# Kernel tuning notes

Measured on AMD Instinct MI355X. Metric: run time of the kernel, lower is better.

The kernel has to match this reference:

```python
import jax, jax.numpy as jnp
import numpy as np

BIG_NUMBER = 1e7   # repo constant used to mask padded adjacency slots
MAX_ITERS = 32     # params['flow_iters']


def _build_graph(B, N, D, valid_deg, seed=0):
    """Random d-regular-ish graph: each valid slot d holds a permutation of nodes,
    so every node has exactly `valid_deg` in-edges. in_indices[b,v,d] = (b,u,s)
    such that adj[b,u,s] == v. Padded slots (d >= valid_deg) hold the sentinel N
    and their in_indices point to a padded (near-zero-weight) flow entry."""
    rng = np.random.default_rng(seed)
    adj = np.full((B, N, D), N, dtype=np.int32)
    in_idx = np.zeros((B, N, D, 3), dtype=np.int32)
    in_idx[..., 0] = np.arange(B, dtype=np.int32)[:, None, None]
    in_idx[..., 2] = valid_deg  # padded slots -> flow[b, 0, valid_deg] (weight ~ 0)
    for b in range(B):
        for d in range(valid_deg):
            perm = rng.permutation(N).astype(np.int32)
            adj[b, :, d] = perm                      # edge u -> perm[u] via slot d
            inv = np.argsort(perm).astype(np.int32)  # inv[v] = u with perm[u] == v
            in_idx[b, :, d, 1] = inv
            in_idx[b, :, d, 2] = d
    return jnp.asarray(adj), jnp.asarray(in_idx)


def setup_inputs():
    B, N, D, VALID = 4, 100000, 16, 12
    key = jax.random.key(0)
    k1, k2 = jax.random.split(key)
    adj_lst, in_indices = _build_graph(B, N, D, VALID)
    return {
        "flow_proportions": jax.random.normal(k1, (B, N, D), dtype=jnp.float32),
        "demands": jax.random.normal(k2, (B, N, 1), dtype=jnp.float32),
        "adj_lst": adj_lst,
        "in_indices": in_indices,
        "num_nodes": N,
    }


def reference(flow_proportions, demands, adj_lst, in_indices, num_nodes):
    # --- masked softmax over neighbor slots (padded slots get -BIG_NUMBER) ---
    mask = (adj_lst == num_nodes).astype(flow_proportions.dtype)   # [B,N,D]
    masked = flow_proportions - BIG_NUMBER * mask
    weights = jax.nn.softmax(masked, axis=-1)                      # normalized_weights

    # --- mcf_solver: iterate flow <- weights * relu(inflow - demand) ---
    bidx = in_indices[..., 0]   # [B,N,D] batch index
    src = in_indices[..., 1]    # [B,N,D] source node of d-th in-edge
    slot = in_indices[..., 2]   # [B,N,D] slot of this node in source's adj list

    def step(flow, _):
        # gather incoming edge flows, sum -> inflow per node [B,N,1]
        inflow = flow[bidx, src, slot].sum(axis=-1, keepdims=True)
        new_flow = weights * jax.nn.relu(inflow - demands)
        return new_flow, None

    flow, _ = jax.lax.scan(step, jnp.zeros_like(weights), None, length=MAX_ITERS)
    # flow_cost (loss) = sum over nodes/slots of cost_fn(flow) = flow**2 here:
    # flow_cost = jnp.sum(flow * flow, axis=(1, 2))
    return flow
```

## Files before the change

### kernel.cpp

```cpp
#include <hip/hip_runtime.h>

#define DEG 16
#define MAX_ITERS 32
#define BLK_F 1024
#define GRID_F 256

__device__ __forceinline__ void grid_barrier(unsigned* cnt, unsigned* gen,
                                             unsigned target, unsigned nblocks) {
    __syncthreads();
    if (threadIdx.x == 0) {
        __threadfence();
        unsigned arrived = __hip_atomic_fetch_add(cnt, 1u, __ATOMIC_ACQ_REL,
                                                  __HIP_MEMORY_SCOPE_AGENT);
        if (arrived == nblocks - 1u) {
            __hip_atomic_store(cnt, 0u, __ATOMIC_RELAXED, __HIP_MEMORY_SCOPE_AGENT);
            __hip_atomic_fetch_add(gen, 1u, __ATOMIC_RELEASE, __HIP_MEMORY_SCOPE_AGENT);
        } else {
            while (__hip_atomic_load(gen, __ATOMIC_RELAXED,
                                     __HIP_MEMORY_SCOPE_AGENT) < target) {
                __builtin_amdgcn_s_sleep(2);
            }
        }
        __threadfence();
    }
    __syncthreads();
}

__device__ __forceinline__ void softmax_row(const float* __restrict__ fp,
                                            const int* __restrict__ adj,
                                            float* __restrict__ wout,
                                            size_t base, int N) {
    const float4* f4 = (const float4*)(fp + base);
    const int4*   a4 = (const int4*)(adj + base);
    float v[DEG];
#pragma unroll
    for (int k = 0; k < DEG / 4; ++k) {
        float4 f = f4[k];
        int4   a = a4[k];
        v[4*k+0] = (a.x == N) ? f.x - 1e7f : f.x;
        v[4*k+1] = (a.y == N) ? f.y - 1e7f : f.y;
        v[4*k+2] = (a.z == N) ? f.z - 1e7f : f.z;
        v[4*k+3] = (a.w == N) ? f.w - 1e7f : f.w;
    }
    float m = v[0];
#pragma unroll
    for (int j = 1; j < DEG; ++j) m = fmaxf(m, v[j]);
    float s = 0.f;
#pragma unroll
    for (int j = 0; j < DEG; ++j) { v[j] = __expf(v[j] - m); s += v[j]; }
    float inv = 1.f / s;
    float4* w4 = (float4*)(wout + base);
#pragma unroll
    for (int k = 0; k < DEG / 4; ++k) {
        float4 o;
        o.x = v[4*k+0] * inv;
        o.y = v[4*k+1] * inv;
        o.z = v[4*k+2] * inv;
        o.w = v[4*k+3] * inv;
        w4[k] = o;
    }
}

__device__ __forceinline__ void load_edges(const int* __restrict__ in_idx,
                                           const float* __restrict__ wsrc,
                                           int n, int N,
                                           int* __restrict__ src,
                                           float* __restrict__ w) {
    const int4* t4 = (const int4*)(in_idx + 3 * (size_t)n * DEG);
#pragma unroll
    for (int g = 0; g < 4; ++g) {
        int4 qa = t4[3*g + 0];
        int4 qb = t4[3*g + 1];
        int4 qc = t4[3*g + 2];
        int b0 = qa.x, s0 = qa.y, l0 = qa.z;
        int b1 = qa.w, s1 = qb.x, l1 = qb.y;
        int b2 = qb.z, s2 = qb.w, l2 = qc.x;
        int b3 = qc.y, s3 = qc.z, l3 = qc.w;
        int f0 = b0 * N + s0, f1 = b1 * N + s1;
        int f2 = b2 * N + s2, f3 = b3 * N + s3;
        src[4*g+0] = f0; src[4*g+1] = f1; src[4*g+2] = f2; src[4*g+3] = f3;
        w[4*g+0] = wsrc[(size_t)f0 * DEG + l0];
        w[4*g+1] = wsrc[(size_t)f1 * DEG + l1];
        w[4*g+2] = wsrc[(size_t)f2 * DEG + l2];
        w[4*g+3] = wsrc[(size_t)f3 * DEG + l3];
    }
}

__global__ __launch_bounds__(BLK_F, 4)
void fused3_k(const float* __restrict__ fp, const int* __restrict__ adj,
              const int* __restrict__ in_idx, const float* __restrict__ dem,
              const int* __restrict__ nn, float* __restrict__ wout,
              float* __restrict__ Ra, float* __restrict__ Rb,
              unsigned* __restrict__ bar_cnt, unsigned* __restrict__ bar_gen,
              int nodes) {
    const int N = *nn;
    const unsigned nb = gridDim.x;
    unsigned bar = 0;

    int start, end;
    if (nodes == 4 * N && nb == GRID_F) {
        int batch = (blockIdx.x & 7) >> 1;
        int rank  = ((blockIdx.x >> 3) << 1) | (blockIdx.x & 1);
        int per   = (N + 63) >> 6;
        int bend  = batch * N + N;
        start = batch * N + rank * per;
        end   = start + per;
        if (end > bend) end = bend;
        if (start > bend) start = bend;
    } else {
        int per = (nodes + nb - 1) / nb;
        start = blockIdx.x * per;
        end   = start + per;
        if (end > nodes) end = nodes;
        if (start > nodes) start = nodes;
    }

    const int n0 = start + (int)threadIdx.x;
    const int n1 = start + (int)threadIdx.x + BLK_F;
    const bool a0 = (n0 < end);
    const bool a1 = (n1 < end);
    const size_t b0 = (size_t)n0 * DEG, b1 = (size_t)n1 * DEG;

    if (a0) softmax_row(fp, adj, wout, b0, N);
    if (a1) softmax_row(fp, adj, wout, b1, N);
    grid_barrier(bar_cnt, bar_gen, ++bar, nb);

    int   src0[DEG], src1[DEG];
    float w0[DEG],   w1[DEG];
    float d0 = 0.f, d1 = 0.f;
#pragma unroll
    for (int k = 0; k < DEG; ++k) { src0[k] = 0; w0[k] = 0.f; src1[k] = 0; w1[k] = 0.f; }
    if (a0) { d0 = dem[n0]; load_edges(in_idx, wout, n0, N, src0, w0); }
    if (a1) { d1 = dem[n1]; load_edges(in_idx, wout, n1, N, src1, w1); }

    unsigned skipA = 0, skipB = 0;
#pragma unroll
    for (int k = 0; k < DEG; ++k) {
        if (__ballot(w0[k] != 0.f) == 0ull) skipA |= (1u << k);
        if (__ballot(w1[k] != 0.f) == 0ull) skipB |= (1u << k);
    }
    const unsigned sk0 = __builtin_amdgcn_readfirstlane(skipA);
    const unsigned sk1 = __builtin_amdgcn_readfirstlane(skipB);

    float r0 = fmaxf(-d0, 0.f), r1 = fmaxf(-d1, 0.f);
    if (a0) Ra[n0] = r0;
    if (a1) Ra[n1] = r1;
    grid_barrier(bar_cnt, bar_gen, ++bar, nb);

    const float* Rin = Ra;
    float*       Rout = Rb;
    for (int t = 1; t < MAX_ITERS; ++t) {
        float acc0 = 0.f, acc1 = 0.f;
        if (a0) {
#pragma unroll
            for (int k = 0; k < DEG; ++k)
                if (!((sk0 >> k) & 1u)) acc0 += w0[k] * Rin[src0[k]];
        }
        if (a1) {
#pragma unroll
            for (int k = 0; k < DEG; ++k)
                if (!((sk1 >> k) & 1u)) acc1 += w1[k] * Rin[src1[k]];
        }
        r0 = fmaxf(acc0 - d0, 0.f);
        r1 = fmaxf(acc1 - d1, 0.f);
        if (t < MAX_ITERS - 1) {
            if (a0) Rout[n0] = r0;
            if (a1) Rout[n1] = r1;
            grid_barrier(bar_cnt, bar_gen, ++bar, nb);
            float* tmp = (float*)Rin; Rin = Rout; Rout = tmp;
        }
    }

    if (a0) {
        float4* w4 = (float4*)(wout + b0);
#pragma unroll
        for (int k = 0; k < DEG / 4; ++k) {
            float4 v = w4[k];
            v.x *= r0; v.y *= r0; v.z *= r0; v.w *= r0;
            w4[k] = v;
        }
    }
    if (a1) {
        float4* w4 = (float4*)(wout + b1);
#pragma unroll
        for (int k = 0; k < DEG / 4; ++k) {
            float4 v = w4[k];
            v.x *= r1; v.y *= r1; v.z *= r1; v.w *= r1;
            w4[k] = v;
        }
    }
}

__global__ void softmax_k(const float* __restrict__ fp, const int* __restrict__ adj,
                          const int* __restrict__ nn, float* __restrict__ wout,
                          int nodes) {
    int i = blockIdx.x * blockDim.x + threadIdx.x;
    if (i >= nodes) return;
    softmax_row(fp, adj, wout, (size_t)i * DEG, *nn);
}

__global__ void gather_k(const int* __restrict__ in_idx, const float* __restrict__ w,
                         const int* __restrict__ nn, int* __restrict__ e_src,
                         float* __restrict__ e_w, int edges) {
    int e = blockIdx.x * blockDim.x + threadIdx.x;
    if (e >= edges) return;
    const int N = *nn;
    size_t e3 = 3 * (size_t)e;
    int fi = in_idx[e3] * N + in_idx[e3 + 1];
    e_src[e] = fi;
    e_w[e]   = w[(size_t)fi * DEG + in_idx[e3 + 2]];
}

__global__ void iter_k(const int* __restrict__ e_src, const float* __restrict__ e_w,
                       const float* __restrict__ dem, const float* __restrict__ Rin,
                       float* __restrict__ Rout, int nodes) {
    int i = blockIdx.x * blockDim.x + threadIdx.x;
    if (i >= nodes) return;
    const size_t base = (size_t)i * DEG;
    const int4*   s4 = (const int4*)(e_src + base);
    const float4* w4 = (const float4*)(e_w + base);
    float acc = 0.f;
#pragma unroll
    for (int k = 0; k < DEG / 4; ++k) {
        int4   s = s4[k];
        float4 w = w4[k];
        acc += w.x * Rin[s.x];
        acc += w.y * Rin[s.y];
        acc += w.z * Rin[s.z];
        acc += w.w * Rin[s.w];
    }
    float r = acc - dem[i];
    Rout[i] = r > 0.f ? r : 0.f;
}

__global__ void final_k(const float* __restrict__ w, const float* __restrict__ R,
                        float* __restrict__ out, int nodes) {
    int i = blockIdx.x * blockDim.x + threadIdx.x;
    if (i >= nodes) return;
    float r = R[i];
    const size_t base = (size_t)i * DEG;
    const float4* w4 = (const float4*)(w + base);
    float4* o4 = (float4*)(out + base);
#pragma unroll
    for (int k = 0; k < DEG / 4; ++k) {
        float4 v = w4[k];
        v.x *= r; v.y *= r; v.z *= r; v.w *= r;
        o4[k] = v;
    }
}

extern "C" void kernel_launch(void* const* d_in, const int* in_sizes, int n_in,
                              void* d_out, int out_size, void* d_ws, size_t ws_size,
                              hipStream_t stream) {
    const float* fp  = (const float*)d_in[0];
    const float* dem = (const float*)d_in[1];
    const int*   adj = (const int*)d_in[2];
    const int*   idx = (const int*)d_in[3];
    const int*   nn  = (const int*)d_in[4];

    const int edges = in_sizes[0];
    const int nodes = in_sizes[1];

    float* weights = (float*)d_out;

    char* ws = (char*)d_ws;
    unsigned* bar_cnt = (unsigned*)ws;
    unsigned* bar_gen = (unsigned*)(ws + 128);
    int*   e_src = (int*)ws;
    float* e_w   = (float*)(ws + (size_t)edges * sizeof(int));
    float* R0    = (float*)(ws + (size_t)edges * sizeof(int) + (size_t)edges * sizeof(float));
    float* R1    = R0 + nodes;

    int dev = 0, cus = 0, maxBlk = 0;
    hipGetDevice(&dev);
    hipDeviceGetAttribute(&cus, hipDeviceAttributeMultiprocessorCount, dev);
    hipOccupancyMaxActiveBlocksPerMultiprocessor(&maxBlk, (const void*)fused3_k,
                                                 BLK_F, 0);

    const int per_blk = (nodes + GRID_F - 1) / GRID_F;

    if (maxBlk >= 1 && cus >= GRID_F && per_blk <= 2 * BLK_F) {
        hipMemsetAsync(ws, 0, 256, stream);
        void* args[] = { (void*)&fp, (void*)&adj, (void*)&idx, (void*)&dem,
                         (void*)&nn, (void*)&weights, (void*)&R0, (void*)&R1,
                         (void*)&bar_cnt, (void*)&bar_gen, (void*)&nodes };
        hipLaunchCooperativeKernel((const void*)fused3_k, dim3(GRID_F), dim3(BLK_F),
                                   args, 0, stream);
    } else {
        const int blk = 256;
        const int gn = (nodes + blk - 1) / blk;
        const int ge = (edges + blk - 1) / blk;
        hipMemsetAsync(R0, 0, (size_t)nodes * sizeof(float), stream);
        softmax_k<<<gn, blk, 0, stream>>>(fp, adj, nn, weights, nodes);
        gather_k<<<ge, blk, 0, stream>>>(idx, weights, nn, e_src, e_w, edges);
        float* a = R0;
        float* b = R1;
        for (int t = 0; t < MAX_ITERS; ++t) {
            iter_k<<<gn, blk, 0, stream>>>(e_src, e_w, dem, a, b, nodes);
            float* tmp = a; a = b; b = tmp;
        }
        final_k<<<gn, blk, 0, stream>>>(weights, a, (float*)d_out, nodes);
    }
}
```

Baseline: 1.029 ms.

## Stage residual vector in LDS chunks instead of random global gathers

Each iteration, the block now cooperatively streams the range of R spanned by its in-edge sources into shared memory in 16K-float chunks, then resolves each edge's gather from LDS. Zero-weight edges are marked with a sentinel, and each thread's edges are bitonic-sorted. The block computes its min/max source range so only the chunks it needs are loaded. This trades scattered global/L2 gathers for coalesced streaming plus extra syncthreads and per-chunk range checks. Random permutation graphs make each block touch nearly its whole batch of R every iteration.

```diff
diff --git a/kernel.cpp b/kernel.cpp
--- a/kernel.cpp
+++ b/kernel.cpp
@@ -4,6 +4,9 @@
 #define MAX_ITERS 32
 #define BLK_F 1024
 #define GRID_F 256
+#define CHUNK_LOG 14
+#define CHUNK (1 << CHUNK_LOG)
+#define SENTINEL 0x7FFFFFFF
 
 __device__ __forceinline__ void grid_barrier(unsigned* cnt, unsigned* gen,
                                              unsigned target, unsigned nblocks) {
@@ -72,12 +75,10 @@
         int4 qa = t4[3*g + 0];
         int4 qb = t4[3*g + 1];
         int4 qc = t4[3*g + 2];
-        int b0 = qa.x, s0 = qa.y, l0 = qa.z;
-        int b1 = qa.w, s1 = qb.x, l1 = qb.y;
-        int b2 = qb.z, s2 = qb.w, l2 = qc.x;
-        int b3 = qc.y, s3 = qc.z, l3 = qc.w;
-        int f0 = b0 * N + s0, f1 = b1 * N + s1;
-        int f2 = b2 * N + s2, f3 = b3 * N + s3;
+        int f0 = qa.x * N + qa.y;  int l0 = qa.z;
+        int f1 = qa.w * N + qb.x;  int l1 = qb.y;
+        int f2 = qb.z * N + qb.w;  int l2 = qc.x;
+        int f3 = qc.y * N + qc.z;  int l3 = qc.w;
         src[4*g+0] = f0; src[4*g+1] = f1; src[4*g+2] = f2; src[4*g+3] = f3;
         w[4*g+0] = wsrc[(size_t)f0 * DEG + l0];
         w[4*g+1] = wsrc[(size_t)f1 * DEG + l1];
@@ -86,13 +87,38 @@
     }
 }
 
+__device__ __forceinline__ void sort16(int* __restrict__ s, float* __restrict__ w) {
+#pragma unroll
+    for (int k = 2; k <= 16; k <<= 1) {
+#pragma unroll
+        for (int j = k >> 1; j > 0; j >>= 1) {
+#pragma unroll
+            for (int i = 0; i < 16; ++i) {
+                int ixj = i ^ j;
+                if (ixj > i) {
+                    const bool up = ((i & k) == 0);
+                    int sa = s[i], sb = s[ixj];
+                    bool sw = up ? (sa > sb) : (sa < sb);
+                    if (sw) {
+                        s[i] = sb; s[ixj] = sa;
+                        float t = w[i]; w[i] = w[ixj]; w[ixj] = t;
+                    }
+                }
+            }
+        }
+    }
+}
+
 __global__ __launch_bounds__(BLK_F, 4)
-void fused3_k(const float* __restrict__ fp, const int* __restrict__ adj,
+void fused5_k(const float* __restrict__ fp, const int* __restrict__ adj,
               const int* __restrict__ in_idx, const float* __restrict__ dem,
               const int* __restrict__ nn, float* __restrict__ wout,
               float* __restrict__ Ra, float* __restrict__ Rb,
               unsigned* __restrict__ bar_cnt, unsigned* __restrict__ bar_gen,
               int nodes) {
+    __shared__ float lds[CHUNK];
+    __shared__ int s_mn, s_mx;
+
     const int N = *nn;
     const unsigned nb = gridDim.x;
     unsigned bar = 0;
@@ -117,8 +143,7 @@
 
     const int n0 = start + (int)threadIdx.x;
     const int n1 = start + (int)threadIdx.x + BLK_F;
-    const bool a0 = (n0 < end);
-    const bool a1 = (n1 < end);
+    const bool a0 = (n0 < end), a1 = (n1 < end);
     const size_t b0 = (size_t)n0 * DEG, b1 = (size_t)n1 * DEG;
 
     if (a0) softmax_row(fp, adj, wout, b0, N);
@@ -129,18 +154,31 @@
     float w0[DEG],   w1[DEG];
     float d0 = 0.f, d1 = 0.f;
 #pragma unroll
-    for (int k = 0; k < DEG; ++k) { src0[k] = 0; w0[k] = 0.f; src1[k] = 0; w1[k] = 0.f; }
+    for (int k = 0; k < DEG; ++k) { src0[k] = SENTINEL; w0[k] = 0.f;
+                                    src1[k] = SENTINEL; w1[k] = 0.f; }
     if (a0) { d0 = dem[n0]; load_edges(in_idx, wout, n0, N, src0, w0); }
     if (a1) { d1 = dem[n1]; load_edges(in_idx, wout, n1, N, src1, w1); }
-
-    unsigned skipA = 0, skipB = 0;
 #pragma unroll
     for (int k = 0; k < DEG; ++k) {
-        if (__ballot(w0[k] != 0.f) == 0ull) skipA |= (1u << k);
-        if (__ballot(w1[k] != 0.f) == 0ull) skipB |= (1u << k);
-    }
-    const unsigned sk0 = __builtin_amdgcn_readfirstlane(skipA);
-    const unsigned sk1 = __builtin_amdgcn_readfirstlane(skipB);
+        if (w0[k] == 0.f) src0[k] = SENTINEL;
+        if (w1[k] == 0.f) src1[k] = SENTINEL;
+    }
+    sort16(src0, w0);
+    sort16(src1, w1);
+
+    int mn = SENTINEL, mx = -1;
+#pragma unroll
+    for (int k = 0; k < DEG; ++k) {
+        if (src0[k] != SENTINEL) { mn = min(mn, src0[k]); mx = max(mx, src0[k]); }
+        if (src1[k] != SENTINEL) { mn = min(mn, src1[k]); mx = max(mx, src1[k]); }
+    }
+    if (threadIdx.x == 0) { s_mn = SENTINEL; s_mx = -1; }
+    __syncthreads();
+    atomicMin(&s_mn, mn);
+    atomicMax(&s_mx, mx);
+    __syncthreads();
+    const int c_lo = (s_mn == SENTINEL) ? 1 : (s_mn >> CHUNK_LOG);
+    const int c_hi = (s_mx < 0) ? 0 : (s_mx >> CHUNK_LOG);
 
     float r0 = fmaxf(-d0, 0.f), r1 = fmaxf(-d1, 0.f);
     if (a0) Ra[n0] = r0;
@@ -151,15 +189,30 @@
     float*       Rout = Rb;
     for (int t = 1; t < MAX_ITERS; ++t) {
         float acc0 = 0.f, acc1 = 0.f;
-        if (a0) {
-#pragma unroll
-            for (int k = 0; k < DEG; ++k)
-                if (!((sk0 >> k) & 1u)) acc0 += w0[k] * Rin[src0[k]];
-        }
-        if (a1) {
-#pragma unroll
-            for (int k = 0; k < DEG; ++k)
-                if (!((sk1 >> k) & 1u)) acc1 += w1[k] * Rin[src1[k]];
+        for (int c = c_lo; c <= c_hi; ++c) {
+            const int cbase = c << CHUNK_LOG;
+#pragma unroll
+            for (int q = 0; q < CHUNK / (BLK_F * 4); ++q) {
+                int li = (q * BLK_F + (int)threadIdx.x) * 4;
+                int gi = cbase + li;
+                if (gi + 4 <= nodes) {
+                    float4 v = *(const float4*)(Rin + gi);
+                    *(float4*)(lds + li) = v;
+                } else {
+#pragma unroll
+                    for (int e = 0; e < 4; ++e)
+                        lds[li + e] = (gi + e < nodes) ? Rin[gi + e] : 0.f;
+                }
+            }
+            __syncthreads();
+#pragma unroll
+            for (int k = 0; k < DEG; ++k) {
+                if ((unsigned)(src0[k] - cbase) < (unsigned)CHUNK)
+                    acc0 += w0[k] * lds[src0[k] - cbase];
+                if ((unsigned)(src1[k] - cbase) < (unsigned)CHUNK)
+                    acc1 += w1[k] * lds[src1[k] - cbase];
+            }
+            __syncthreads();
         }
         r0 = fmaxf(acc0 - d0, 0.f);
         r1 = fmaxf(acc1 - d1, 0.f);
@@ -266,6 +319,8 @@
     char* ws = (char*)d_ws;
     unsigned* bar_cnt = (unsigned*)ws;
     unsigned* bar_gen = (unsigned*)(ws + 128);
+    float* R0f = (float*)(ws + 256);
+    float* R1f = R0f + nodes;
     int*   e_src = (int*)ws;
     float* e_w   = (float*)(ws + (size_t)edges * sizeof(int));
     float* R0    = (float*)(ws + (size_t)edges * sizeof(int) + (size_t)edges * sizeof(float));
@@ -274,7 +329,7 @@
     int dev = 0, cus = 0, maxBlk = 0;
     hipGetDevice(&dev);
     hipDeviceGetAttribute(&cus, hipDeviceAttributeMultiprocessorCount, dev);
-    hipOccupancyMaxActiveBlocksPerMultiprocessor(&maxBlk, (const void*)fused3_k,
+    hipOccupancyMaxActiveBlocksPerMultiprocessor(&maxBlk, (const void*)fused5_k,
                                                  BLK_F, 0);
 
     const int per_blk = (nodes + GRID_F - 1) / GRID_F;
@@ -282,9 +337,9 @@
     if (maxBlk >= 1 && cus >= GRID_F && per_blk <= 2 * BLK_F) {
         hipMemsetAsync(ws, 0, 256, stream);
         void* args[] = { (void*)&fp, (void*)&adj, (void*)&idx, (void*)&dem,
-                         (void*)&nn, (void*)&weights, (void*)&R0, (void*)&R1,
+                         (void*)&nn, (void*)&weights, (void*)&R0f, (void*)&R1f,
                          (void*)&bar_cnt, (void*)&bar_gen, (void*)&nodes };
-        hipLaunchCooperativeKernel((const void*)fused3_k, dim3(GRID_F), dim3(BLK_F),
+        hipLaunchCooperativeKernel((const void*)fused5_k, dim3(GRID_F), dim3(BLK_F),
                                    args, 0, stream);
     } else {
         const int blk = 256;
```

New measurement: 1.026 ms. No clear change (-0.2%).
